# Performance work log

Measured on AMD Instinct MI355X. Metric: run time of the kernel, lower is better.

The kernel has to match this reference:

```python
import jax, jax.numpy as jnp
import numpy as np

B, HW, ENC, DEC, ATTN = 512, 196, 2048, 512, 512

def setup_inputs() -> dict:
    key = jax.random.key(0)
    ks = jax.random.split(key, 8)
    s_enc = 1.0 / np.sqrt(ENC)
    s_dec = 1.0 / np.sqrt(DEC)
    s_v = 1.0 / np.sqrt(ATTN)
    return {
        "enc_out": jax.random.normal(ks[0], (B, HW, ENC), dtype=jnp.float32),
        "dec_h": jax.random.normal(ks[1], (B, DEC), dtype=jnp.float32),
        "W_enc": jax.random.uniform(ks[2], (ENC, ATTN), jnp.float32, -s_enc, s_enc),
        "b_enc": jax.random.uniform(ks[3], (ATTN,), jnp.float32, -s_enc, s_enc),
        "W_dec": jax.random.uniform(ks[4], (DEC, ATTN), jnp.float32, -s_dec, s_dec),
        "b_dec": jax.random.uniform(ks[5], (ATTN,), jnp.float32, -s_dec, s_dec),
        "W_v": jax.random.uniform(ks[6], (ATTN,), jnp.float32, -s_v, s_v),
        "b_v": jax.random.uniform(ks[7], (), jnp.float32, -s_v, s_v),
    }

def reference(enc_out, dec_h, W_enc, b_enc, W_dec, b_dec, W_v, b_v):
    # attn1: [B, HW, ATTN]; attn2: [B, 1, ATTN]
    attn1 = jnp.einsum('bse,ea->bsa', enc_out, W_enc) + b_enc
    attn2 = (dec_h @ W_dec + b_dec)[:, None, :]
    score = jax.nn.relu(attn1 + attn2)
    logits = jnp.einsum('bsa,a->bs', score, W_v) + b_v  # [B, HW]
    alpha = jax.nn.softmax(logits, axis=1)
    context_vec = jnp.einsum('bs,bse->be', alpha, enc_out)
    return (context_vec, alpha)
```

## Files before the change

kernel.cpp:

```cpp
#include <hip/hip_runtime.h>
#include <hip/hip_bf16.h>
#include <cstdint>
#include <cstddef>

#define B_    512
#define HW_   196
#define ENC_  2048
#define DEC_  512
#define ATTN_ 512
#define M_    (B_*HW_)

typedef __attribute__((ext_vector_type(8))) short short8;
typedef __attribute__((ext_vector_type(4))) float f32x4;

__device__ __forceinline__ unsigned short f2bf(float x) {
  union { float f; unsigned int u; } c; c.f = x;
  unsigned int u = c.u;
  return (unsigned short)((u + 0x7FFFu + ((u >> 16) & 1u)) >> 16);
}

__device__ __forceinline__ void gload_lds16(const void* g, void* l) {
  __builtin_amdgcn_global_load_lds(
      (const __attribute__((address_space(1))) void*)g,
      (__attribute__((address_space(3))) void*)l, 16, 0, 0);
}

__global__ __launch_bounds__(256)
void k_attn2(const float* __restrict__ dec_h, const float* __restrict__ Wdec,
             const float* __restrict__ bdec, const float* __restrict__ benc,
             float* __restrict__ attn2p) {
  __shared__ float dh[DEC_];
  const int b = blockIdx.x;
  const int t = threadIdx.x;
  dh[t]       = dec_h[b*DEC_ + t];
  dh[t + 256] = dec_h[b*DEC_ + t + 256];
  __syncthreads();
  #pragma unroll
  for (int rep = 0; rep < 2; ++rep) {
    const int a = t + rep*256;
    float acc = bdec[a] + benc[a];
    #pragma unroll 8
    for (int k = 0; k < DEC_; ++k)
      acc = fmaf(dh[k], Wdec[(size_t)k*ATTN_ + a], acc);
    attn2p[(size_t)b*ATTN_ + a] = acc;
  }
}

__global__ __launch_bounds__(256)
void k_transpose(const float* __restrict__ Wenc, unsigned short* __restrict__ WencT) {
  __shared__ float tile[32][33];
  const int e0 = blockIdx.x * 32;
  const int a0 = blockIdx.y * 32;
  const int t  = threadIdx.x;
  const int li = t >> 5;
  const int lj = t & 31;
  #pragma unroll
  for (int rep = 0; rep < 4; ++rep) {
    const int i = li + rep*8;
    tile[i][lj] = Wenc[(size_t)(e0 + i)*ATTN_ + a0 + lj];
  }
  __syncthreads();
  #pragma unroll
  for (int rep = 0; rep < 4; ++rep) {
    const int ar = li + rep*8;
    WencT[(size_t)(a0 + ar)*ENC_ + e0 + lj] = f2bf(tile[lj][ar]);
  }
}

#define BM 128
#define BN 128
#define BK 32
#define LDA 40
#define NT (ENC_/BK)

__global__ __launch_bounds__(256)
void k_gemm_logits(const float* __restrict__ enc,
                   const unsigned short* __restrict__ WencT,
                   const float* __restrict__ attn2p,
                   const float* __restrict__ Wv,
                   float* __restrict__ partials) {
  __shared__ unsigned short As[BM*LDA];
  __shared__ unsigned short Bs[2][BN*BK];
  __shared__ float plog[BM][2];

  const int tid  = threadIdx.x;
  const int id   = blockIdx.x;
  const int xcd  = id & 7;
  const int rest = id >> 3;
  const int nb   = rest & 3;
  const int mblk = (rest >> 2) * 8 + xcd;
  const int r0 = mblk * BM;
  const int n0 = nb * BN;

  const int arow  = tid >> 1;
  const int ahalf = (tid & 1) << 4;
  const float* aptr = enc + (size_t)(r0 + arow)*ENC_ + ahalf;

  const unsigned short* bbase = WencT + (size_t)n0*ENC_;

  const int w  = tid >> 6;
  const int l  = tid & 63;
  const int wm = w >> 1, wn = w & 1;
  const int lrow = l & 15;
  const int lk8  = (l >> 4) << 3;
  const int g4   = (l >> 4) << 2;

  f32x4 acc[4][4];
  #pragma unroll
  for (int mi = 0; mi < 4; ++mi)
    #pragma unroll
    for (int ni = 0; ni < 4; ++ni)
      acc[mi][ni] = (f32x4){0.f, 0.f, 0.f, 0.f};

  float4 ar[4];
  #pragma unroll
  for (int i = 0; i < 4; ++i) ar[i] = *reinterpret_cast<const float4*>(aptr + i*4);
  #pragma unroll
  for (int r = 0; r < 2; ++r) {
    const int idx = r*256 + tid;
    gload_lds16(bbase + (size_t)(idx >> 2)*ENC_ + (idx & 3)*8, &Bs[0][idx*8]);
  }

  for (int kt = 0; kt < NT; ++kt) {
    {
      unsigned int pk[8];
      #pragma unroll
      for (int i = 0; i < 4; ++i) {
        pk[2*i]   = (unsigned)f2bf(ar[i].x) | ((unsigned)f2bf(ar[i].y) << 16);
        pk[2*i+1] = (unsigned)f2bf(ar[i].z) | ((unsigned)f2bf(ar[i].w) << 16);
      }
      uint4* da = reinterpret_cast<uint4*>(&As[arow*LDA + ahalf]);
      da[0] = make_uint4(pk[0], pk[1], pk[2], pk[3]);
      da[1] = make_uint4(pk[4], pk[5], pk[6], pk[7]);
    }
    __syncthreads();

    if (kt + 1 < NT) {
      const float* ap = aptr + (kt + 1)*BK;
      #pragma unroll
      for (int i = 0; i < 4; ++i) ar[i] = *reinterpret_cast<const float4*>(ap + i*4);
      const int k0n = (kt + 1)*BK;
      unsigned short* bdst = Bs[(kt + 1) & 1];
      #pragma unroll
      for (int r = 0; r < 2; ++r) {
        const int idx = r*256 + tid;
        gload_lds16(bbase + (size_t)(idx >> 2)*ENC_ + k0n + (idx & 3)*8, &bdst[idx*8]);
      }
    }

    const unsigned short* bsc = Bs[kt & 1];
    short8 aF[4], bF[4];
    #pragma unroll
    for (int mi = 0; mi < 4; ++mi)
      aF[mi] = *reinterpret_cast<const short8*>(&As[(wm*64 + mi*16 + lrow)*LDA + lk8]);
    #pragma unroll
    for (int ni = 0; ni < 4; ++ni)
      bF[ni] = *reinterpret_cast<const short8*>(&bsc[(wn*64 + ni*16 + lrow)*BK + lk8]);
    #pragma unroll
    for (int mi = 0; mi < 4; ++mi)
      #pragma unroll
      for (int ni = 0; ni < 4; ++ni)
        acc[mi][ni] = __builtin_amdgcn_mfma_f32_16x16x32_bf16(aF[mi], bF[ni], acc[mi][ni], 0, 0, 0);
    __syncthreads();
  }

  float wvv[4];
  #pragma unroll
  for (int ni = 0; ni < 4; ++ni) wvv[ni] = Wv[n0 + wn*64 + ni*16 + lrow];
  #pragma unroll
  for (int mi = 0; mi < 4; ++mi) {
    #pragma unroll
    for (int j = 0; j < 4; ++j) {
      const int row_local = wm*64 + mi*16 + g4 + j;
      const int r  = r0 + row_local;
      const int bb = r / HW_;
      const float* a2 = attn2p + (size_t)bb*ATTN_ + n0 + wn*64;
      float s = 0.f;
      #pragma unroll
      for (int ni = 0; ni < 4; ++ni) {
        float v = acc[mi][ni][j] + a2[ni*16 + lrow];
        v = fmaxf(v, 0.f);
        s = fmaf(v, wvv[ni], s);
      }
      s += __shfl_xor(s, 1);
      s += __shfl_xor(s, 2);
      s += __shfl_xor(s, 4);
      s += __shfl_xor(s, 8);
      if (lrow == 0) plog[row_local][wn] = s;
    }
  }
  __syncthreads();
  if (tid < BM)
    partials[(size_t)(r0 + tid)*4 + nb] = plog[tid][0] + plog[tid][1];
}

__global__ __launch_bounds__(64)
void k_softmax(const float* __restrict__ partials, const float* __restrict__ bvp,
               float* __restrict__ alpha) {
  const int b = blockIdx.x;
  const int t = threadIdx.x;
  const float bv = bvp[0];
  float lg[4];
  #pragma unroll
  for (int i = 0; i < 4; ++i) {
    const int s = t + i*64;
    if (s < HW_) {
      const float4 p = *reinterpret_cast<const float4*>(&partials[(size_t)(b*HW_ + s)*4]);
      lg[i] = p.x + p.y + p.z + p.w + bv;
    } else lg[i] = -INFINITY;
  }
  float mx = fmaxf(fmaxf(lg[0], lg[1]), fmaxf(lg[2], lg[3]));
  #pragma unroll
  for (int off = 32; off; off >>= 1) mx = fmaxf(mx, __shfl_xor(mx, off));
  float sum = 0.f;
  #pragma unroll
  for (int i = 0; i < 4; ++i) { lg[i] = expf(lg[i] - mx); sum += lg[i]; }
  #pragma unroll
  for (int off = 32; off; off >>= 1) sum += __shfl_xor(sum, off);
  const float inv = 1.0f / sum;
  #pragma unroll
  for (int i = 0; i < 4; ++i) {
    const int s = t + i*64;
    if (s < HW_) alpha[b*HW_ + s] = lg[i] * inv;
  }
}

__global__ __launch_bounds__(256)
void k_context(const float* __restrict__ enc, const float* __restrict__ alpha,
               float* __restrict__ ctx) {
  __shared__ float al[HW_];
  const int bi = blockIdx.x;
  const int b  = bi >> 1;
  const int e0 = (bi & 1) << 10;
  const int t  = threadIdx.x;
  if (t < HW_) al[t] = alpha[b*HW_ + t];
  __syncthreads();
  const float* base = enc + (size_t)b*HW_*ENC_ + e0 + t*4;
  float4 acc = {0.f, 0.f, 0.f, 0.f};
  #pragma unroll 4
  for (int s = 0; s < HW_; ++s) {
    const float a = al[s];
    const float4 v = *reinterpret_cast<const float4*>(base + (size_t)s*ENC_);
    acc.x = fmaf(a, v.x, acc.x);
    acc.y = fmaf(a, v.y, acc.y);
    acc.z = fmaf(a, v.z, acc.z);
    acc.w = fmaf(a, v.w, acc.w);
  }
  *reinterpret_cast<float4*>(&ctx[(size_t)b*ENC_ + e0 + t*4]) = acc;
}

extern "C" void kernel_launch(void* const* d_in, const int* in_sizes, int n_in,
                              void* d_out, int out_size, void* d_ws, size_t ws_size,
                              hipStream_t stream) {
  const float* enc   = (const float*)d_in[0];
  const float* dec_h = (const float*)d_in[1];
  const float* Wenc  = (const float*)d_in[2];
  const float* benc  = (const float*)d_in[3];
  const float* Wdec  = (const float*)d_in[4];
  const float* bdec  = (const float*)d_in[5];
  const float* Wv    = (const float*)d_in[6];
  const float* bv    = (const float*)d_in[7];

  float* ctx   = (float*)d_out;
  float* alpha = (float*)d_out + (size_t)B_*ENC_;

  char* ws = (char*)d_ws;
  float*          attn2p   = (float*)ws;
  unsigned short* WencT    = (unsigned short*)(ws + (1u << 20));
  float*          partials = (float*)(ws + 3u*(1u << 20));

  hipLaunchKernelGGL(k_attn2,     dim3(B_),               dim3(256), 0, stream,
                     dec_h, Wdec, bdec, benc, attn2p);
  hipLaunchKernelGGL(k_transpose, dim3(ENC_/32, ATTN_/32), dim3(256), 0, stream,
                     Wenc, WencT);
  hipLaunchKernelGGL(k_gemm_logits, dim3(3136),           dim3(256), 0, stream,
                     enc, WencT, attn2p, Wv, partials);
  hipLaunchKernelGGL(k_softmax,   dim3(B_),               dim3(64),  0, stream,
                     partials, bv, alpha);
  hipLaunchKernelGGL(k_context,   dim3(1024),             dim3(256), 0, stream,
                     enc, alpha, ctx);
}
```

Baseline: 684.4 us.

## Stage fp32 encoder tiles directly into LDS with triple-buffered async GEMM pipeline

The logits GEMM now loads fp32 encoder tiles straight into LDS with global_load_lds instead of going through registers, and converts them to bf16 when building the MFMA fragments. Both A and B tiles are triple-buffered with XOR-swizzled layouts, explicit vmcnt waits and one barrier per k-step, and MFMA issue gets raised priority via setprio. The aim is to overlap global loads with compute and drop the register round-trip and the extra barrier of the old double-buffered scheme. In exchange the kernel uses more LDS (fp32 A tiles, three stages), repeats the bf16 conversion per wave, and relies on hand-written waitcnt logic.

```diff
diff --git a/kernel.cpp b/kernel.cpp
--- a/kernel.cpp
+++ b/kernel.cpp
@@ -14,9 +14,11 @@
 typedef __attribute__((ext_vector_type(4))) float f32x4;
 
 __device__ __forceinline__ unsigned short f2bf(float x) {
-  union { float f; unsigned int u; } c; c.f = x;
-  unsigned int u = c.u;
-  return (unsigned short)((u + 0x7FFFu + ((u >> 16) & 1u)) >> 16);
+  __bf16 b = (__bf16)x;
+  return __builtin_bit_cast(unsigned short, b);
+}
+__device__ __forceinline__ unsigned int cvt2(float x, float y) {
+  return (unsigned)f2bf(x) | ((unsigned)f2bf(y) << 16);
 }
 
 __device__ __forceinline__ void gload_lds16(const void* g, void* l) {
@@ -67,43 +69,62 @@
   }
 }
 
-#define BM 128
-#define BN 128
-#define BK 32
-#define LDA 40
-#define NT (ENC_/BK)
-
-__global__ __launch_bounds__(256)
-void k_gemm_logits(const float* __restrict__ enc,
-                   const unsigned short* __restrict__ WencT,
-                   const float* __restrict__ attn2p,
-                   const float* __restrict__ Wv,
-                   float* __restrict__ partials) {
-  __shared__ unsigned short As[BM*LDA];
-  __shared__ unsigned short Bs[2][BN*BK];
-  __shared__ float plog[BM][2];
-
-  const int tid  = threadIdx.x;
-  const int id   = blockIdx.x;
+#define NKS 64
+
+__global__ __launch_bounds__(256, 2)
+void k_gemm_f32(const float* __restrict__ enc,
+                const unsigned short* __restrict__ WencT,
+                const float* __restrict__ attn2p,
+                const float* __restrict__ Wv,
+                float* __restrict__ partials) {
+  __shared__ float          A3[3][128*32];
+  __shared__ unsigned short B3[3][128*32];
+
+  const int tid = threadIdx.x;
+  const int id  = blockIdx.x;
   const int xcd  = id & 7;
   const int rest = id >> 3;
   const int nb   = rest & 3;
-  const int mblk = (rest >> 2) * 8 + xcd;
-  const int r0 = mblk * BM;
-  const int n0 = nb * BN;
-
-  const int arow  = tid >> 1;
-  const int ahalf = (tid & 1) << 4;
-  const float* aptr = enc + (size_t)(r0 + arow)*ENC_ + ahalf;
-
-  const unsigned short* bbase = WencT + (size_t)n0*ENC_;
+  const int mblk = (rest >> 2)*8 + xcd;
+  const int r0 = mblk * 128;
+  const int n0 = nb * 128;
 
   const int w  = tid >> 6;
   const int l  = tid & 63;
   const int wm = w >> 1, wn = w & 1;
   const int lrow = l & 15;
-  const int lk8  = (l >> 4) << 3;
-  const int g4   = (l >> 4) << 2;
+  const int kg   = l >> 4;
+
+  const float* aSrc[4];
+  #pragma unroll
+  for (int i = 0; i < 4; ++i) {
+    const int j  = tid + i*256;
+    const int rr = j >> 3;
+    const int c  = (j & 7) ^ (rr & 7);
+    aSrc[i] = enc + (size_t)(r0 + rr)*ENC_ + c*4;
+  }
+  const unsigned short* bSrc[2];
+  #pragma unroll
+  for (int i = 0; i < 2; ++i) {
+    const int j  = tid + i*256;
+    const int rr = j >> 2;
+    const int kc = (j & 3) ^ ((rr >> 1) & 3);
+    bSrc[i] = WencT + (size_t)(n0 + rr)*ENC_ + kc*8;
+  }
+
+  int aOffF[4][2];
+  #pragma unroll
+  for (int mi = 0; mi < 4; ++mi) {
+    const int R = wm*64 + mi*16 + lrow;
+    aOffF[mi][0] = (R*8 + ((2*kg)     ^ (R & 7))) * 4;
+    aOffF[mi][1] = (R*8 + ((2*kg + 1) ^ (R & 7))) * 4;
+  }
+  int bOff[4];
+  #pragma unroll
+  for (int ni = 0; ni < 4; ++ni) {
+    const int C = wn*64 + ni*16 + lrow;
+    bOff[ni] = (C*4 + (kg ^ ((C >> 1) & 3))) * 8;
+  }
 
   f32x4 acc[4][4];
   #pragma unroll
@@ -112,58 +133,58 @@
     for (int ni = 0; ni < 4; ++ni)
       acc[mi][ni] = (f32x4){0.f, 0.f, 0.f, 0.f};
 
-  float4 ar[4];
-  #pragma unroll
-  for (int i = 0; i < 4; ++i) ar[i] = *reinterpret_cast<const float4*>(aptr + i*4);
-  #pragma unroll
-  for (int r = 0; r < 2; ++r) {
-    const int idx = r*256 + tid;
-    gload_lds16(bbase + (size_t)(idx >> 2)*ENC_ + (idx & 3)*8, &Bs[0][idx*8]);
-  }
-
-  for (int kt = 0; kt < NT; ++kt) {
-    {
-      unsigned int pk[8];
-      #pragma unroll
-      for (int i = 0; i < 4; ++i) {
-        pk[2*i]   = (unsigned)f2bf(ar[i].x) | ((unsigned)f2bf(ar[i].y) << 16);
-        pk[2*i+1] = (unsigned)f2bf(ar[i].z) | ((unsigned)f2bf(ar[i].w) << 16);
-      }
-      uint4* da = reinterpret_cast<uint4*>(&As[arow*LDA + ahalf]);
-      da[0] = make_uint4(pk[0], pk[1], pk[2], pk[3]);
-      da[1] = make_uint4(pk[4], pk[5], pk[6], pk[7]);
+#define STAGE(KT) do {                                                         \
+    const size_t _ko = (size_t)(KT)*32;                                        \
+    const int _bw = (KT) % 3;                                                  \
+    gload_lds16(aSrc[0] + _ko, &A3[_bw][tid*4]);                               \
+    gload_lds16(aSrc[1] + _ko, &A3[_bw][1024 + tid*4]);                        \
+    gload_lds16(aSrc[2] + _ko, &A3[_bw][2048 + tid*4]);                        \
+    gload_lds16(aSrc[3] + _ko, &A3[_bw][3072 + tid*4]);                        \
+    gload_lds16(bSrc[0] + _ko, &B3[_bw][tid*8]);                               \
+    gload_lds16(bSrc[1] + _ko, &B3[_bw][2048 + tid*8]);                        \
+  } while (0)
+
+  STAGE(0); STAGE(1);
+  asm volatile("s_waitcnt vmcnt(6)" ::: "memory");
+  __builtin_amdgcn_s_barrier();
+
+  for (int kt = 0; kt < NKS; ++kt) {
+    const float*          aB = &A3[kt % 3][0];
+    const unsigned short* bB = &B3[kt % 3][0];
+
+    __builtin_amdgcn_s_setprio(1);
+    short8 aF[4], bF[4];
+    #pragma unroll
+    for (int mi = 0; mi < 4; ++mi) {
+      const f32x4 a0 = *reinterpret_cast<const f32x4*>(&aB[aOffF[mi][0]]);
+      const f32x4 a1 = *reinterpret_cast<const f32x4*>(&aB[aOffF[mi][1]]);
+      uint4 pk;
+      pk.x = cvt2(a0.x, a0.y);  pk.y = cvt2(a0.z, a0.w);
+      pk.z = cvt2(a1.x, a1.y);  pk.w = cvt2(a1.z, a1.w);
+      aF[mi] = __builtin_bit_cast(short8, pk);
     }
-    __syncthreads();
-
-    if (kt + 1 < NT) {
-      const float* ap = aptr + (kt + 1)*BK;
-      #pragma unroll
-      for (int i = 0; i < 4; ++i) ar[i] = *reinterpret_cast<const float4*>(ap + i*4);
-      const int k0n = (kt + 1)*BK;
-      unsigned short* bdst = Bs[(kt + 1) & 1];
-      #pragma unroll
-      for (int r = 0; r < 2; ++r) {
-        const int idx = r*256 + tid;
-        gload_lds16(bbase + (size_t)(idx >> 2)*ENC_ + k0n + (idx & 3)*8, &bdst[idx*8]);
-      }
-    }
-
-    const unsigned short* bsc = Bs[kt & 1];
-    short8 aF[4], bF[4];
-    #pragma unroll
-    for (int mi = 0; mi < 4; ++mi)
-      aF[mi] = *reinterpret_cast<const short8*>(&As[(wm*64 + mi*16 + lrow)*LDA + lk8]);
     #pragma unroll
     for (int ni = 0; ni < 4; ++ni)
-      bF[ni] = *reinterpret_cast<const short8*>(&bsc[(wn*64 + ni*16 + lrow)*BK + lk8]);
+      bF[ni] = *reinterpret_cast<const short8*>(&bB[bOff[ni]]);
     #pragma unroll
     for (int mi = 0; mi < 4; ++mi)
       #pragma unroll
       for (int ni = 0; ni < 4; ++ni)
-        acc[mi][ni] = __builtin_amdgcn_mfma_f32_16x16x32_bf16(aF[mi], bF[ni], acc[mi][ni], 0, 0, 0);
-    __syncthreads();
-  }
-
+        acc[mi][ni] = __builtin_amdgcn_mfma_f32_16x16x32_bf16(
+            aF[mi], bF[ni], acc[mi][ni], 0, 0, 0);
+    __builtin_amdgcn_s_setprio(0);
+
+    if (kt + 2 < NKS) STAGE(kt + 2);
+
+    asm volatile("s_waitcnt lgkmcnt(0)" ::: "memory");
+    if (kt <= NKS - 3)      { asm volatile("s_waitcnt vmcnt(6)" ::: "memory"); }
+    else if (kt == NKS - 2) { asm volatile("s_waitcnt vmcnt(0)" ::: "memory"); }
+    __builtin_amdgcn_s_barrier();
+  }
+#undef STAGE
+
+  __syncthreads();
+  float* plog = reinterpret_cast<float*>(&A3[0][0]);
   float wvv[4];
   #pragma unroll
   for (int ni = 0; ni < 4; ++ni) wvv[ni] = Wv[n0 + wn*64 + ni*16 + lrow];
@@ -171,7 +192,7 @@
   for (int mi = 0; mi < 4; ++mi) {
     #pragma unroll
     for (int j = 0; j < 4; ++j) {
-      const int row_local = wm*64 + mi*16 + g4 + j;
+      const int row_local = wm*64 + mi*16 + kg*4 + j;
       const int r  = r0 + row_local;
       const int bb = r / HW_;
       const float* a2 = attn2p + (size_t)bb*ATTN_ + n0 + wn*64;
@@ -186,17 +207,17 @@
       s += __shfl_xor(s, 2);
       s += __shfl_xor(s, 4);
       s += __shfl_xor(s, 8);
-      if (lrow == 0) plog[row_local][wn] = s;
+      if (lrow == 0) plog[row_local*2 + wn] = s;
     }
   }
   __syncthreads();
-  if (tid < BM)
-    partials[(size_t)(r0 + tid)*4 + nb] = plog[tid][0] + plog[tid][1];
+  if (tid < 128)
+    partials[(size_t)(r0 + tid)*4 + nb] = plog[tid*2] + plog[tid*2 + 1];
 }
 
 __global__ __launch_bounds__(64)
-void k_softmax(const float* __restrict__ partials, const float* __restrict__ bvp,
-               float* __restrict__ alpha) {
+void k_softmax4(const float* __restrict__ partials, const float* __restrict__ bvp,
+                float* __restrict__ alpha) {
   const int b = blockIdx.x;
   const int t = threadIdx.x;
   const float bv = bvp[0];
@@ -226,8 +247,8 @@
 }
 
 __global__ __launch_bounds__(256)
-void k_context(const float* __restrict__ enc, const float* __restrict__ alpha,
-               float* __restrict__ ctx) {
+void k_context_f32(const float* __restrict__ enc, const float* __restrict__ alpha,
+                   float* __restrict__ ctx) {
   __shared__ float al[HW_];
   const int bi = blockIdx.x;
   const int b  = bi >> 1;
@@ -269,14 +290,14 @@
   unsigned short* WencT    = (unsigned short*)(ws + (1u << 20));
   float*          partials = (float*)(ws + 3u*(1u << 20));
 
-  hipLaunchKernelGGL(k_attn2,     dim3(B_),               dim3(256), 0, stream,
+  hipLaunchKernelGGL(k_attn2,      dim3(B_),                dim3(256), 0, stream,
                      dec_h, Wdec, bdec, benc, attn2p);
-  hipLaunchKernelGGL(k_transpose, dim3(ENC_/32, ATTN_/32), dim3(256), 0, stream,
+  hipLaunchKernelGGL(k_transpose,  dim3(ENC_/32, ATTN_/32), dim3(256), 0, stream,
                      Wenc, WencT);
-  hipLaunchKernelGGL(k_gemm_logits, dim3(3136),           dim3(256), 0, stream,
+  hipLaunchKernelGGL(k_gemm_f32,   dim3(3136),              dim3(256), 0, stream,
                      enc, WencT, attn2p, Wv, partials);
-  hipLaunchKernelGGL(k_softmax,   dim3(B_),               dim3(64),  0, stream,
+  hipLaunchKernelGGL(k_softmax4,   dim3(B_),                dim3(64),  0, stream,
                      partials, bv, alpha);
-  hipLaunchKernelGGL(k_context,   dim3(1024),             dim3(256), 0, stream,
+  hipLaunchKernelGGL(k_context_f32, dim3(1024),             dim3(256), 0, stream,
                      enc, alpha, ctx);
 }
```

Result: slower. 712.2 us (+4.1%).
